# Performance work log

Hardware: AMD Instinct MI355X
Metric: run time of the kernel (lower is better)

Reference implementation:

```python
import jax, jax.numpy as jnp
import numpy as np

HIDDEN = 128
EDGE_DIM = 64
N_NODES = 50000
N_EDGES = 600000

def _linear_params(key, fan_in, fan_out):
    kw, kb = jax.random.split(key)
    bound = 1.0 / np.sqrt(fan_in)
    W = jax.random.uniform(kw, (fan_in, fan_out), minval=-bound, maxval=bound, dtype=jnp.float32)
    b = jax.random.uniform(kb, (fan_out,), minval=-bound, maxval=bound, dtype=jnp.float32)
    return W, b

def setup_inputs() -> dict:
    key = jax.random.key(0)
    ks = jax.random.split(key, 10)
    h = jax.random.normal(ks[0], (N_NODES, HIDDEN), dtype=jnp.float32)
    edge_index = jax.random.randint(ks[1], (2, N_EDGES), 0, N_NODES, dtype=jnp.int64)
    edge_attr = jax.random.normal(ks[2], (N_EDGES, EDGE_DIM), dtype=jnp.float32)
    mW1, mb1 = _linear_params(ks[3], 2 * HIDDEN + EDGE_DIM, HIDDEN)
    mW2, mb2 = _linear_params(ks[4], HIDDEN, HIDDEN)
    mW3, mb3 = _linear_params(ks[5], HIDDEN, HIDDEN)
    uW1, ub1 = _linear_params(ks[6], 2 * HIDDEN, HIDDEN)
    uW2, ub2 = _linear_params(ks[7], HIDDEN, HIDDEN)
    gamma = jnp.ones((HIDDEN,), dtype=jnp.float32)
    beta = jnp.zeros((HIDDEN,), dtype=jnp.float32)
    return {"h": h, "edge_index": edge_index, "edge_attr": edge_attr,
            "mW1": mW1, "mb1": mb1, "mW2": mW2, "mb2": mb2, "mW3": mW3, "mb3": mb3,
            "uW1": uW1, "ub1": ub1, "uW2": uW2, "ub2": ub2,
            "gamma": gamma, "beta": beta}

def reference(h, edge_index, edge_attr, mW1, mb1, mW2, mb2, mW3, mb3, uW1, ub1, uW2, ub2, gamma, beta):
    src, dst = edge_index[0], edge_index[1]
    # message MLP on [E, 2*H + edge_dim]
    x = jnp.concatenate([h[src], h[dst], edge_attr], axis=-1)
    x = jax.nn.gelu(x @ mW1 + mb1)
    x = jax.nn.gelu(x @ mW2 + mb2)
    msgs = x @ mW3 + mb3  # [E, H]
    # scatter-mean aggregate to destination nodes
    agg = jax.ops.segment_sum(msgs, dst, num_segments=h.shape[0])
    count = jax.ops.segment_sum(jnp.ones((dst.shape[0], 1), dtype=h.dtype), dst, num_segments=h.shape[0])
    agg = agg / (count + 1e-8)
    # update MLP
    u = jnp.concatenate([h, agg], axis=-1)
    u = jax.nn.gelu(u @ uW1 + ub1)
    out = u @ uW2 + ub2
    # LayerNorm(out + h)
    y = out + h
    mu = jnp.mean(y, axis=-1, keepdims=True)
    var = jnp.var(y, axis=-1, keepdims=True)
    return (y - mu) / jnp.sqrt(var + 1e-5) * gamma + beta
```

## Files before the change

### kernel.cpp

```cpp
#include <hip/hip_runtime.h>

#define E_TOTAL 600000
#define NN 50000

typedef _Float16 half8 __attribute__((ext_vector_type(8)));
typedef _Float16 half2v __attribute__((ext_vector_type(2)));
typedef float float4v __attribute__((ext_vector_type(4)));
typedef float float2v __attribute__((ext_vector_type(2)));

__device__ __forceinline__ float gelu_tanh(float x) {
    float u = 0.7978845608028654f * (x + 0.044715f * x * x * x);
    float ex = __expf(2.0f * u);
    float t = 1.0f - 2.0f / (ex + 1.0f);
    return 0.5f * x * (1.0f + t);
}

__device__ __forceinline__ int act_idx(int c, int row, int q) {
    int idx = ((c * 128 + row) << 3) + q;
    idx ^= ((row >> 3) & 3) << 4;
    idx ^= (c & 1) << 3;
    return idx;
}
__device__ __forceinline__ int act_idx64(int c, int row, int q) {
    int idx = ((c * 64 + row) << 3) + q;
    idx ^= ((row >> 3) & 3) << 4;
    idx ^= (c & 1) << 3;
    return idx;
}

__device__ __forceinline__ half8 cvt8(float4v x0, float4v x1) {
    half8 a;
    a[0] = (_Float16)x0[0]; a[1] = (_Float16)x0[1]; a[2] = (_Float16)x0[2]; a[3] = (_Float16)x0[3];
    a[4] = (_Float16)x1[0]; a[5] = (_Float16)x1[1]; a[6] = (_Float16)x1[2]; a[7] = (_Float16)x1[3];
    return a;
}

__global__ __launch_bounds__(256) void pack_all(
    const float* __restrict__ mW1, const float* __restrict__ mW2, const float* __restrict__ mW3,
    const float* __restrict__ uW1, const float* __restrict__ uW2,
    _Float16* __restrict__ dst)
{
    int t = blockIdx.x * 256 + threadIdx.x;
    const float* src;
    int loc;
    if (t < 40960)        { src = mW1; loc = t; }
    else if (t < 57344)   { src = mW2; loc = t - 40960; }
    else if (t < 73728)   { src = mW3; loc = t - 57344; }
    else if (t < 106496)  { src = uW1; loc = t - 73728; }
    else if (t < 122880)  { src = uW2; loc = t - 106496; }
    else return;
    int i   = loc & 7;
    int col = (loc >> 3) & 127;
    int c   = loc >> 10;
    dst[t] = (_Float16)src[(8 * c + i) * 128 + col];
}

__global__ __launch_bounds__(256) void cvt_pre(
    const float* __restrict__ h, const float* __restrict__ ea,
    _Float16* __restrict__ hf, _Float16* __restrict__ ef)
{
    const int stride = gridDim.x * 256;
    for (int i = blockIdx.x * 256 + threadIdx.x; i < 5600000; i += stride) {
        if (i < 800000) {
            float4v a = ((const float4v*)h)[2 * i];
            float4v b = ((const float4v*)h)[2 * i + 1];
            ((half8*)hf)[i] = cvt8(a, b);
        } else {
            int j = i - 800000;
            float4v a = ((const float4v*)ea)[2 * j];
            float4v b = ((const float4v*)ea)[2 * j + 1];
            ((half8*)ef)[j] = cvt8(a, b);
        }
    }
}

__device__ __forceinline__ int detect_i64(const int* ei) {
    int allz = 1;
    #pragma unroll
    for (int j = 1; j < 64; j += 2) allz &= (ei[j] == 0);
    return allz;
}

__global__ __launch_bounds__(256) void count_kernel(const int* __restrict__ ei, int* __restrict__ cnt_i) {
    __shared__ int s_mode;
    if (threadIdx.x == 0) s_mode = detect_i64(ei);
    __syncthreads();
    int e = blockIdx.x * 256 + threadIdx.x;
    if (e >= E_TOTAL) return;
    int d = s_mode ? (int)((const long long*)ei)[E_TOTAL + e] : ei[E_TOTAL + e];
    atomicAdd(&cnt_i[d], 1);
}

__global__ __launch_bounds__(1024) void scan_kernel(const int* __restrict__ cnt_i, int* __restrict__ offs) {
    __shared__ int part[1024];
    const int t = threadIdx.x;
    const int PER = (NN + 1023) / 1024;
    const int base = t * PER;
    int s = 0;
    for (int j = 0; j < PER; ++j) { int idx = base + j; if (idx < NN) s += cnt_i[idx]; }
    part[t] = s;
    __syncthreads();
    for (int off = 1; off < 1024; off <<= 1) {
        int v = (t >= off) ? part[t - off] : 0;
        __syncthreads();
        part[t] += v;
        __syncthreads();
    }
    int run = (t == 0) ? 0 : part[t - 1];
    for (int j = 0; j < PER; ++j) { int idx = base + j; if (idx < NN) { offs[idx] = run; run += cnt_i[idx]; } }
    if (t == 1023) offs[NN] = part[1023];
}

__global__ __launch_bounds__(256) void fill_kernel(const int* __restrict__ ei, const int* __restrict__ offs,
                                                   int* __restrict__ cursor, int* __restrict__ perm) {
    __shared__ int s_mode;
    if (threadIdx.x == 0) s_mode = detect_i64(ei);
    __syncthreads();
    int e = blockIdx.x * 256 + threadIdx.x;
    if (e >= E_TOTAL) return;
    int d = s_mode ? (int)((const long long*)ei)[E_TOTAL + e] : ei[E_TOTAL + e];
    int pos = offs[d] + atomicAdd(&cursor[d], 1);
    perm[pos] = e;
}

__global__ __launch_bounds__(256) void agg_kernel(const _Float16* __restrict__ msgs,
                                                  const int* __restrict__ offs, const int* __restrict__ perm,
                                                  float* __restrict__ agg, float* __restrict__ cntf) {
    const int node = blockIdx.x * 4 + (threadIdx.x >> 6);
    const int l = threadIdx.x & 63;
    const int beg = offs[node], end = offs[node + 1];
    float2v s = {0.0f, 0.0f};
    const half2v* base = (const half2v*)msgs;
    for (int j = beg; j < end; ++j) {
        const int e = perm[j];
        half2v v = __builtin_nontemporal_load(&base[(size_t)e * 64 + l]);
        s.x += (float)v[0]; s.y += (float)v[1];
    }
    ((float2v*)agg)[(size_t)node * 64 + l] = s;
    if (l == 0) cntf[node] = (float)(end - beg);
}

template<int ATOMIC>
__global__ __launch_bounds__(128, 3) void msg_kernel(
    const _Float16* __restrict__ hf16, const int* __restrict__ ei, const _Float16* __restrict__ ef16,
    const _Float16* __restrict__ pw1, const _Float16* __restrict__ pw2, const _Float16* __restrict__ pw3,
    const float* __restrict__ mb1, const float* __restrict__ mb2, const float* __restrict__ mb3,
    _Float16* __restrict__ msgs, float* __restrict__ agg, float* __restrict__ cnt)
{
    __shared__ int s_src[64];
    __shared__ int s_dst[64];
    __shared__ int s_mode;
    __shared__ __align__(16) _Float16 s_act[16 * 64 * 8];

    const int tid = threadIdx.x;
    const int e0  = blockIdx.x * 64;

    if (tid == 0) s_mode = detect_i64(ei);
    __syncthreads();

    if (tid < 64) {
        int e = e0 + tid;
        int srcn, dstn;
        if (s_mode) {
            const long long* e64 = (const long long*)ei;
            srcn = (int)e64[e];
            dstn = (int)e64[E_TOTAL + e];
        } else {
            srcn = ei[e];
            dstn = ei[E_TOTAL + e];
        }
        s_src[tid] = srcn;
        s_dst[tid] = dstn;
        if (ATOMIC) unsafeAtomicAdd(&cnt[dstn], 1.0f);
    }
    __syncthreads();

    const int w = tid >> 6, l = tid & 63, lhi = l >> 4, llo = l & 15;
    const int r0 = 32 * w;
    const float4v fzero = {0.0f, 0.0f, 0.0f, 0.0f};

    const _Float16* srcP[2];
    const _Float16* dstP[2];
    const _Float16* eP[2];
    #pragma unroll
    for (int ms = 0; ms < 2; ++ms) {
        const int row = r0 + 16 * ms + llo;
        srcP[ms] = hf16 + (size_t)s_src[row] * 128 + 8 * lhi;
        dstP[ms] = hf16 + (size_t)s_dst[row] * 128 + 8 * lhi;
        eP[ms]   = ef16 + (size_t)(e0 + row) * 64 + 8 * lhi;
    }

    float4v acc[2][8];
    #pragma unroll
    for (int ms = 0; ms < 2; ++ms)
        #pragma unroll
        for (int t = 0; t < 8; ++t) acc[ms][t] = fzero;

    half8 af[4][2];
    #pragma unroll
    for (int s = 0; s < 4; ++s)
        #pragma unroll
        for (int ms = 0; ms < 2; ++ms)
            af[s][ms] = *(const half8*)(srcP[ms] + 32 * s);

    #pragma unroll
    for (int s = 0; s < 10; ++s) {
        const int bbase = ((4 * s + lhi) * 128 + llo) << 3;
        #pragma unroll
        for (int t = 0; t < 8; ++t) {
            const half8 b = *(const half8*)(pw1 + bbase + (t << 7));
            acc[0][t] = __builtin_amdgcn_mfma_f32_16x16x32_f16(af[s & 3][0], b, acc[0][t], 0, 0, 0);
            acc[1][t] = __builtin_amdgcn_mfma_f32_16x16x32_f16(af[s & 3][1], b, acc[1][t], 0, 0, 0);
        }
        if (s + 4 <= 9) {
            const int sn = s + 4;
            #pragma unroll
            for (int ms = 0; ms < 2; ++ms) {
                const _Float16* p;
                if (sn < 8) p = dstP[ms] + 32 * (sn - 4);
                else        p = eP[ms] + 32 * (sn - 8);
                af[sn & 3][ms] = *(const half8*)p;
            }
        }
    }

    #pragma unroll
    for (int t = 0; t < 8; ++t) {
        const int col = 16 * t + llo;
        const float b1 = mb1[col];
        #pragma unroll
        for (int ms = 0; ms < 2; ++ms)
            #pragma unroll
            for (int i = 0; i < 4; ++i) {
                const int row = r0 + 16 * ms + 4 * lhi + i;
                float v = gelu_tanh(acc[ms][t][i] + b1);
                s_act[act_idx64(col >> 3, row, col & 7)] = (_Float16)v;
            }
    }

    float4v acc2[2][8];
    #pragma unroll
    for (int ms = 0; ms < 2; ++ms)
        #pragma unroll
        for (int t = 0; t < 8; ++t) acc2[ms][t] = fzero;

    #pragma unroll
    for (int s = 0; s < 4; ++s) {
        half8 a2[2];
        #pragma unroll
        for (int ms = 0; ms < 2; ++ms)
            a2[ms] = *(const half8*)&s_act[act_idx64(4 * s + lhi, r0 + 16 * ms + llo, 0)];
        const int bbase = ((4 * s + lhi) * 128 + llo) << 3;
        #pragma unroll
        for (int t = 0; t < 8; ++t) {
            const half8 b = *(const half8*)(pw2 + bbase + (t << 7));
            acc2[0][t] = __builtin_amdgcn_mfma_f32_16x16x32_f16(a2[0], b, acc2[0][t], 0, 0, 0);
            acc2[1][t] = __builtin_amdgcn_mfma_f32_16x16x32_f16(a2[1], b, acc2[1][t], 0, 0, 0);
        }
    }

    #pragma unroll
    for (int t = 0; t < 8; ++t) {
        const int col = 16 * t + llo;
        const float b2 = mb2[col];
        #pragma unroll
        for (int ms = 0; ms < 2; ++ms)
            #pragma unroll
            for (int i = 0; i < 4; ++i) {
                const int row = r0 + 16 * ms + 4 * lhi + i;
                float v = gelu_tanh(acc2[ms][t][i] + b2);
                s_act[act_idx64(col >> 3, row, col & 7)] = (_Float16)v;
            }
    }

    float4v acc3[2][8];
    #pragma unroll
    for (int ms = 0; ms < 2; ++ms)
        #pragma unroll
        for (int t = 0; t < 8; ++t) acc3[ms][t] = fzero;

    #pragma unroll
    for (int s = 0; s < 4; ++s) {
        half8 a3[2];
        #pragma unroll
        for (int ms = 0; ms < 2; ++ms)
            a3[ms] = *(const half8*)&s_act[act_idx64(4 * s + lhi, r0 + 16 * ms + llo, 0)];
        const int bbase = ((4 * s + lhi) * 128 + llo) << 3;
        #pragma unroll
        for (int t = 0; t < 8; ++t) {
            const half8 b = *(const half8*)(pw3 + bbase + (t << 7));
            acc3[0][t] = __builtin_amdgcn_mfma_f32_16x16x32_f16(a3[0], b, acc3[0][t], 0, 0, 0);
            acc3[1][t] = __builtin_amdgcn_mfma_f32_16x16x32_f16(a3[1], b, acc3[1][t], 0, 0, 0);
        }
    }

    float mb3v[8];
    #pragma unroll
    for (int t = 0; t < 8; ++t) mb3v[t] = mb3[16 * t + llo];

    #pragma unroll
    for (int ms = 0; ms < 2; ++ms)
        #pragma unroll
        for (int i = 0; i < 4; ++i) {
            const int row = r0 + 16 * ms + 4 * lhi + i;
            if (ATOMIC) {
                const size_t dbase = (size_t)s_dst[row] * 128;
                #pragma unroll
                for (int t = 0; t < 8; ++t)
                    unsafeAtomicAdd(&agg[dbase + 16 * t + llo], acc3[ms][t][i] + mb3v[t]);
            } else {
                _Float16* mrow = msgs + (size_t)(e0 + row) * 128;
                #pragma unroll
                for (int t = 0; t < 8; ++t)
                    __builtin_nontemporal_store((_Float16)(acc3[ms][t][i] + mb3v[t]), mrow + 16 * t + llo);
            }
        }
}

__global__ __launch_bounds__(256) void upd_kernel(
    const float* __restrict__ h, const _Float16* __restrict__ hf16,
    const _Float16* __restrict__ pu1, const _Float16* __restrict__ pu2,
    const float* __restrict__ ub1, const float* __restrict__ ub2,
    const float* __restrict__ gamma, const float* __restrict__ beta,
    const float* __restrict__ agg, const float* __restrict__ cnt,
    float* __restrict__ out)
{
    __shared__ __align__(16) _Float16 s_act[16 * 128 * 8];

    const int tid = threadIdx.x;
    const int n0  = blockIdx.x * 128;
    const int w = tid >> 6, l = tid & 63, lhi = l >> 4, llo = l & 15;
    const int r0 = 32 * w;
    const float4v fzero = {0.0f, 0.0f, 0.0f, 0.0f};

    float rcp[2];
    size_t nodeOff[2];
    #pragma unroll
    for (int ms = 0; ms < 2; ++ms) {
        int node = n0 + r0 + 16 * ms + llo;
        if (node >= NN) node = NN - 1;
        nodeOff[ms] = (size_t)node * 128;
        rcp[ms] = 1.0f / (cnt[node] + 1e-8f);
    }

    float4v acc[2][8];
    #pragma unroll
    for (int ms = 0; ms < 2; ++ms)
        #pragma unroll
        for (int t = 0; t < 8; ++t) acc[ms][t] = fzero;

    #pragma unroll
    for (int s = 0; s < 8; ++s) {
        half8 af[2];
        #pragma unroll
        for (int ms = 0; ms < 2; ++ms) {
            if (s < 4) {
                af[ms] = *(const half8*)(hf16 + nodeOff[ms] + 32 * s + 8 * lhi);
            } else {
                const float* p = agg + nodeOff[ms] + 32 * (s - 4) + 8 * lhi;
                float4v x0 = *(const float4v*)p;
                float4v x1 = *(const float4v*)(p + 4);
                x0 *= rcp[ms]; x1 *= rcp[ms];
                af[ms] = cvt8(x0, x1);
            }
        }
        const int bbase = ((4 * s + lhi) * 128 + llo) << 3;
        #pragma unroll
        for (int t = 0; t < 8; ++t) {
            const half8 b = *(const half8*)(pu1 + bbase + (t << 7));
            acc[0][t] = __builtin_amdgcn_mfma_f32_16x16x32_f16(af[0], b, acc[0][t], 0, 0, 0);
            acc[1][t] = __builtin_amdgcn_mfma_f32_16x16x32_f16(af[1], b, acc[1][t], 0, 0, 0);
        }
    }

    #pragma unroll
    for (int t = 0; t < 8; ++t) {
        const int col = 16 * t + llo;
        const float b1 = ub1[col];
        #pragma unroll
        for (int ms = 0; ms < 2; ++ms)
            #pragma unroll
            for (int i = 0; i < 4; ++i) {
                const int row = r0 + 16 * ms + 4 * lhi + i;
                float v = gelu_tanh(acc[ms][t][i] + b1);
                s_act[act_idx(col >> 3, row, col & 7)] = (_Float16)v;
            }
    }

    float4v acc2[2][8];
    #pragma unroll
    for (int ms = 0; ms < 2; ++ms)
        #pragma unroll
        for (int t = 0; t < 8; ++t) acc2[ms][t] = fzero;

    #pragma unroll
    for (int s = 0; s < 4; ++s) {
        half8 af[2];
        #pragma unroll
        for (int ms = 0; ms < 2; ++ms)
            af[ms] = *(const half8*)&s_act[act_idx(4 * s + lhi, r0 + 16 * ms + llo, 0)];
        const int bbase = ((4 * s + lhi) * 128 + llo) << 3;
        #pragma unroll
        for (int t = 0; t < 8; ++t) {
            const half8 b = *(const half8*)(pu2 + bbase + (t << 7));
            acc2[0][t] = __builtin_amdgcn_mfma_f32_16x16x32_f16(af[0], b, acc2[0][t], 0, 0, 0);
            acc2[1][t] = __builtin_amdgcn_mfma_f32_16x16x32_f16(af[1], b, acc2[1][t], 0, 0, 0);
        }
    }

    float ub2v[8], gv[8], bv[8];
    #pragma unroll
    for (int t = 0; t < 8; ++t) {
        const int col = 16 * t + llo;
        ub2v[t] = ub2[col]; gv[t] = gamma[col]; bv[t] = beta[col];
    }

    #pragma unroll
    for (int ms = 0; ms < 2; ++ms)
        #pragma unroll
        for (int i = 0; i < 4; ++i) {
            const int noderow = n0 + r0 + 16 * ms + 4 * lhi + i;
            const int nodec = noderow < NN ? noderow : NN - 1;
            float y[8];
            float sum = 0.0f;
            #pragma unroll
            for (int t = 0; t < 8; ++t) {
                const int col = 16 * t + llo;
                float v = acc2[ms][t][i] + ub2v[t] + h[(size_t)nodec * 128 + col];
                y[t] = v; sum += v;
            }
            sum += __shfl_xor(sum, 1, 16);
            sum += __shfl_xor(sum, 2, 16);
            sum += __shfl_xor(sum, 4, 16);
            sum += __shfl_xor(sum, 8, 16);
            const float mu = sum * (1.0f / 128.0f);
            float sq = 0.0f;
            #pragma unroll
            for (int t = 0; t < 8; ++t) { float d = y[t] - mu; sq += d * d; }
            sq += __shfl_xor(sq, 1, 16);
            sq += __shfl_xor(sq, 2, 16);
            sq += __shfl_xor(sq, 4, 16);
            sq += __shfl_xor(sq, 8, 16);
            const float rs = rsqrtf(sq * (1.0f / 128.0f) + 1e-5f);
            if (noderow < NN) {
                #pragma unroll
                for (int t = 0; t < 8; ++t) {
                    const int col = 16 * t + llo;
                    out[(size_t)noderow * 128 + col] = (y[t] - mu) * rs * gv[t] + bv[t];
                }
            }
        }
}

extern "C" void kernel_launch(void* const* d_in, const int* in_sizes, int n_in,
                              void* d_out, int out_size, void* d_ws, size_t ws_size,
                              hipStream_t stream) {
    const float* h     = (const float*)d_in[0];
    const int*   ei    = (const int*)d_in[1];
    const float* eattr = (const float*)d_in[2];
    const float* mW1   = (const float*)d_in[3];
    const float* mb1   = (const float*)d_in[4];
    const float* mW2   = (const float*)d_in[5];
    const float* mb2   = (const float*)d_in[6];
    const float* mW3   = (const float*)d_in[7];
    const float* mb3   = (const float*)d_in[8];
    const float* uW1   = (const float*)d_in[9];
    const float* ub1   = (const float*)d_in[10];
    const float* uW2   = (const float*)d_in[11];
    const float* ub2   = (const float*)d_in[12];
    const float* gamma = (const float*)d_in[13];
    const float* beta  = (const float*)d_in[14];
    float* out = (float*)d_out;

    char* ws = (char*)d_ws;

    const size_t OFF_MSGS = 0;
    const size_t OFF_AGG  = 153600000;
    const size_t OFF_HF   = 179200000;
    const size_t OFF_EF   = 192000000;
    const size_t OFF_CNTI = 268800000;
    const size_t OFF_CURS = 269000000;
    const size_t OFF_OFFS = 269200000;
    const size_t OFF_PERM = 269400064;
    const size_t OFF_CNTF = 271800064;
    const size_t OFF_PW   = 272000064;
    const size_t NEED     = 272245824;

    if (ws_size >= NEED) {
        _Float16* msgs  = (_Float16*)(ws + OFF_MSGS);
        float* agg      = (float*)(ws + OFF_AGG);
        _Float16* hf16  = (_Float16*)(ws + OFF_HF);
        _Float16* ef16  = (_Float16*)(ws + OFF_EF);
        int* cnt_i      = (int*)(ws + OFF_CNTI);
        int* cursor     = (int*)(ws + OFF_CURS);
        int* offs       = (int*)(ws + OFF_OFFS);
        int* perm       = (int*)(ws + OFF_PERM);
        float* cntf     = (float*)(ws + OFF_CNTF);
        _Float16* pw    = (_Float16*)(ws + OFF_PW);
        _Float16* pw1 = pw;
        _Float16* pw2 = pw + 40960;
        _Float16* pw3 = pw + 57344;
        _Float16* pu1 = pw + 73728;
        _Float16* pu2 = pw + 106496;

        hipMemsetAsync(ws + OFF_CNTI, 0, 400000, stream);

        pack_all<<<480, 256, 0, stream>>>(mW1, mW2, mW3, uW1, uW2, pw);
        cvt_pre<<<2048, 256, 0, stream>>>(h, eattr, hf16, ef16);
        count_kernel<<<(E_TOTAL + 255) / 256, 256, 0, stream>>>(ei, cnt_i);
        scan_kernel<<<1, 1024, 0, stream>>>(cnt_i, offs);
        fill_kernel<<<(E_TOTAL + 255) / 256, 256, 0, stream>>>(ei, offs, cursor, perm);

        msg_kernel<0><<<E_TOTAL / 64, 128, 0, stream>>>(
            hf16, ei, ef16, pw1, pw2, pw3, mb1, mb2, mb3, msgs, nullptr, nullptr);

        agg_kernel<<<NN / 4, 256, 0, stream>>>(msgs, offs, perm, agg, cntf);

        upd_kernel<<<(NN + 127) / 128, 256, 0, stream>>>(
            h, hf16, pu1, pu2, ub1, ub2, gamma, beta, agg, cntf, out);
    } else {
        float* agg     = (float*)ws;
        float* cnt     = (float*)(ws + 25600000);
        _Float16* hf16 = (_Float16*)(ws + 25800000);
        _Float16* ef16 = (_Float16*)(ws + 38600000);
        _Float16* pw   = (_Float16*)(ws + 115400000);
        _Float16* pw1 = pw;
        _Float16* pw2 = pw + 40960;
        _Float16* pw3 = pw + 57344;
        _Float16* pu1 = pw + 73728;
        _Float16* pu2 = pw + 106496;

        hipMemsetAsync(ws, 0, 25800000, stream);

        pack_all<<<480, 256, 0, stream>>>(mW1, mW2, mW3, uW1, uW2, pw);
        cvt_pre<<<2048, 256, 0, stream>>>(h, eattr, hf16, ef16);

        msg_kernel<1><<<E_TOTAL / 64, 128, 0, stream>>>(
            hf16, ei, ef16, pw1, pw2, pw3, mb1, mb2, mb3, nullptr, agg, cnt);

        upd_kernel<<<(NN + 127) / 128, 256, 0, stream>>>(
            h, hf16, pu1, pu2, ub1, ub2, gamma, beta, agg, cnt, out);
    }
}
```

Baseline: 858.2 us.

## Process edges in destination-sorted order and read fp32 edge attributes directly

```diff
diff --git a/kernel.cpp b/kernel.cpp
--- a/kernel.cpp
+++ b/kernel.cpp
@@ -56,21 +56,13 @@
 }
 
 __global__ __launch_bounds__(256) void cvt_pre(
-    const float* __restrict__ h, const float* __restrict__ ea,
-    _Float16* __restrict__ hf, _Float16* __restrict__ ef)
+    const float* __restrict__ h, _Float16* __restrict__ hf)
 {
     const int stride = gridDim.x * 256;
-    for (int i = blockIdx.x * 256 + threadIdx.x; i < 5600000; i += stride) {
-        if (i < 800000) {
-            float4v a = ((const float4v*)h)[2 * i];
-            float4v b = ((const float4v*)h)[2 * i + 1];
-            ((half8*)hf)[i] = cvt8(a, b);
-        } else {
-            int j = i - 800000;
-            float4v a = ((const float4v*)ea)[2 * j];
-            float4v b = ((const float4v*)ea)[2 * j + 1];
-            ((half8*)ef)[j] = cvt8(a, b);
-        }
+    for (int i = blockIdx.x * 256 + threadIdx.x; i < 800000; i += stride) {
+        float4v a = ((const float4v*)h)[2 * i];
+        float4v b = ((const float4v*)h)[2 * i + 1];
+        ((half8*)hf)[i] = cvt8(a, b);
     }
 }
 
@@ -124,16 +116,24 @@
 }
 
 __global__ __launch_bounds__(256) void agg_kernel(const _Float16* __restrict__ msgs,
-                                                  const int* __restrict__ offs, const int* __restrict__ perm,
+                                                  const int* __restrict__ offs,
                                                   float* __restrict__ agg, float* __restrict__ cntf) {
     const int node = blockIdx.x * 4 + (threadIdx.x >> 6);
     const int l = threadIdx.x & 63;
     const int beg = offs[node], end = offs[node + 1];
     float2v s = {0.0f, 0.0f};
-    const half2v* base = (const half2v*)msgs;
-    for (int j = beg; j < end; ++j) {
-        const int e = perm[j];
-        half2v v = __builtin_nontemporal_load(&base[(size_t)e * 64 + l]);
+    const half2v* p = (const half2v*)msgs + (size_t)beg * 64 + l;
+    int j = beg;
+    for (; j + 3 < end; j += 4, p += 256) {
+        half2v a = __builtin_nontemporal_load(p);
+        half2v b = __builtin_nontemporal_load(p + 64);
+        half2v c = __builtin_nontemporal_load(p + 128);
+        half2v d = __builtin_nontemporal_load(p + 192);
+        s.x += (float)a[0] + (float)b[0] + (float)c[0] + (float)d[0];
+        s.y += (float)a[1] + (float)b[1] + (float)c[1] + (float)d[1];
+    }
+    for (; j < end; ++j, p += 64) {
+        half2v v = __builtin_nontemporal_load(p);
         s.x += (float)v[0]; s.y += (float)v[1];
     }
     ((float2v*)agg)[(size_t)node * 64 + l] = s;
@@ -142,11 +142,13 @@
 
 template<int ATOMIC>
 __global__ __launch_bounds__(128, 3) void msg_kernel(
-    const _Float16* __restrict__ hf16, const int* __restrict__ ei, const _Float16* __restrict__ ef16,
+    const _Float16* __restrict__ hf16, const int* __restrict__ ei, const float* __restrict__ eattr,
+    const int* __restrict__ perm,
     const _Float16* __restrict__ pw1, const _Float16* __restrict__ pw2, const _Float16* __restrict__ pw3,
     const float* __restrict__ mb1, const float* __restrict__ mb2, const float* __restrict__ mb3,
     _Float16* __restrict__ msgs, float* __restrict__ agg, float* __restrict__ cnt)
 {
+    __shared__ int s_e[64];
     __shared__ int s_src[64];
     __shared__ int s_dst[64];
     __shared__ int s_mode;
@@ -159,7 +161,8 @@
     __syncthreads();
 
     if (tid < 64) {
-        int e = e0 + tid;
+        int e = perm[e0 + tid];
+        s_e[tid] = e;
         int srcn, dstn;
         if (s_mode) {
             const long long* e64 = (const long long*)ei;
@@ -181,13 +184,13 @@
 
     const _Float16* srcP[2];
     const _Float16* dstP[2];
-    const _Float16* eP[2];
+    const float*    eP[2];
     #pragma unroll
     for (int ms = 0; ms < 2; ++ms) {
         const int row = r0 + 16 * ms + llo;
         srcP[ms] = hf16 + (size_t)s_src[row] * 128 + 8 * lhi;
         dstP[ms] = hf16 + (size_t)s_dst[row] * 128 + 8 * lhi;
-        eP[ms]   = ef16 + (size_t)(e0 + row) * 64 + 8 * lhi;
+        eP[ms]   = eattr + (size_t)s_e[row] * 64 + 8 * lhi;
     }
 
     float4v acc[2][8];
@@ -216,10 +219,14 @@
             const int sn = s + 4;
             #pragma unroll
             for (int ms = 0; ms < 2; ++ms) {
-                const _Float16* p;
-                if (sn < 8) p = dstP[ms] + 32 * (sn - 4);
-                else        p = eP[ms] + 32 * (sn - 8);
-                af[sn & 3][ms] = *(const half8*)p;
+                if (sn < 8) {
+                    af[sn & 3][ms] = *(const half8*)(dstP[ms] + 32 * (sn - 4));
+                } else {
+                    const float* p = eP[ms] + 32 * (sn - 8);
+                    float4v x0 = *(const float4v*)p;
+                    float4v x1 = *(const float4v*)(p + 4);
+                    af[sn & 3][ms] = cvt8(x0, x1);
+                }
             }
         }
     }
@@ -477,20 +484,18 @@
     const size_t OFF_MSGS = 0;
     const size_t OFF_AGG  = 153600000;
     const size_t OFF_HF   = 179200000;
-    const size_t OFF_EF   = 192000000;
-    const size_t OFF_CNTI = 268800000;
-    const size_t OFF_CURS = 269000000;
-    const size_t OFF_OFFS = 269200000;
-    const size_t OFF_PERM = 269400064;
-    const size_t OFF_CNTF = 271800064;
-    const size_t OFF_PW   = 272000064;
-    const size_t NEED     = 272245824;
+    const size_t OFF_CNTI = 192000000;
+    const size_t OFF_CURS = 192200000;
+    const size_t OFF_OFFS = 192400000;
+    const size_t OFF_PERM = 192600064;
+    const size_t OFF_CNTF = 195000064;
+    const size_t OFF_PW   = 195200064;
+    const size_t NEED     = 195445824;
 
     if (ws_size >= NEED) {
         _Float16* msgs  = (_Float16*)(ws + OFF_MSGS);
         float* agg      = (float*)(ws + OFF_AGG);
         _Float16* hf16  = (_Float16*)(ws + OFF_HF);
-        _Float16* ef16  = (_Float16*)(ws + OFF_EF);
         int* cnt_i      = (int*)(ws + OFF_CNTI);
         int* cursor     = (int*)(ws + OFF_CURS);
         int* offs       = (int*)(ws + OFF_OFFS);
@@ -505,16 +510,16 @@
 
         hipMemsetAsync(ws + OFF_CNTI, 0, 400000, stream);
 
-        pack_all<<<480, 256, 0, stream>>>(mW1, mW2, mW3, uW1, uW2, pw);
-        cvt_pre<<<2048, 256, 0, stream>>>(h, eattr, hf16, ef16);
         count_kernel<<<(E_TOTAL + 255) / 256, 256, 0, stream>>>(ei, cnt_i);
         scan_kernel<<<1, 1024, 0, stream>>>(cnt_i, offs);
         fill_kernel<<<(E_TOTAL + 255) / 256, 256, 0, stream>>>(ei, offs, cursor, perm);
+        pack_all<<<480, 256, 0, stream>>>(mW1, mW2, mW3, uW1, uW2, pw);
+        cvt_pre<<<1024, 256, 0, stream>>>(h, hf16);
 
         msg_kernel<0><<<E_TOTAL / 64, 128, 0, stream>>>(
-            hf16, ei, ef16, pw1, pw2, pw3, mb1, mb2, mb3, msgs, nullptr, nullptr);
-
-        agg_kernel<<<NN / 4, 256, 0, stream>>>(msgs, offs, perm, agg, cntf);
+            hf16, ei, eattr, perm, pw1, pw2, pw3, mb1, mb2, mb3, msgs, nullptr, nullptr);
+
+        agg_kernel<<<NN / 4, 256, 0, stream>>>(msgs, offs, agg, cntf);
 
         upd_kernel<<<(NN + 127) / 128, 256, 0, stream>>>(
             h, hf16, pu1, pu2, ub1, ub2, gamma, beta, agg, cntf, out);
@@ -522,8 +527,11 @@
         float* agg     = (float*)ws;
         float* cnt     = (float*)(ws + 25600000);
         _Float16* hf16 = (_Float16*)(ws + 25800000);
-        _Float16* ef16 = (_Float16*)(ws + 38600000);
-        _Float16* pw   = (_Float16*)(ws + 115400000);
+        int* cnt_i     = (int*)(ws + 38600000);
+        int* cursor    = (int*)(ws + 38800000);
+        int* offs      = (int*)(ws + 39000000);
+        int* perm      = (int*)(ws + 39200064);
+        _Float16* pw   = (_Float16*)(ws + 41600064);
         _Float16* pw1 = pw;
         _Float16* pw2 = pw + 40960;
         _Float16* pw3 = pw + 57344;
@@ -531,12 +539,16 @@
         _Float16* pu2 = pw + 106496;
 
         hipMemsetAsync(ws, 0, 25800000, stream);
-
+        hipMemsetAsync(ws + 38600000, 0, 400000, stream);
+
+        count_kernel<<<(E_TOTAL + 255) / 256, 256, 0, stream>>>(ei, cnt_i);
+        scan_kernel<<<1, 1024, 0, stream>>>(cnt_i, offs);
+        fill_kernel<<<(E_TOTAL + 255) / 256, 256, 0, stream>>>(ei, offs, cursor, perm);
         pack_all<<<480, 256, 0, stream>>>(mW1, mW2, mW3, uW1, uW2, pw);
-        cvt_pre<<<2048, 256, 0, stream>>>(h, eattr, hf16, ef16);
+        cvt_pre<<<1024, 256, 0, stream>>>(h, hf16);
 
         msg_kernel<1><<<E_TOTAL / 64, 128, 0, stream>>>(
-            hf16, ei, ef16, pw1, pw2, pw3, mb1, mb2, mb3, nullptr, agg, cnt);
+            hf16, ei, eattr, perm, pw1, pw2, pw3, mb1, mb2, mb3, nullptr, agg, cnt);
 
         upd_kernel<<<(NN + 127) / 128, 256, 0, stream>>>(
             h, hf16, pu1, pu2, ub1, ub2, gamma, beta, agg, cnt, out);
```

Result: faster. 755.5 us (-12.0%).
